# Performance work log

Hardware: AMD Instinct MI355X
Metric: run time of the kernel (lower is better)

## Reference

```python
import jax, jax.numpy as jnp
import numpy as np
import math

D_MODEL = 512
N_HEADS = 8
D_HEAD = D_MODEL // N_HEADS
B, T = 2, 2048


def quant_linear(x, W, b, bitwidth):
    # BitNet-b1.58 style: ternary weights (per-tensor absmean scale),
    # activations quantized to signed `bitwidth` with per-token absmax scale.
    ws = jnp.mean(jnp.abs(W)) + 1e-5
    Wq = jnp.clip(jnp.round(W / ws), -1.0, 1.0)
    Qb = 2.0 ** (bitwidth - 1) - 1.0
    xs = Qb / (jnp.max(jnp.abs(x), axis=-1, keepdims=True) + 1e-5)
    xq = jnp.clip(jnp.round(x * xs), -Qb, Qb)
    return (xq @ W.T if False else jnp.einsum('...i,oi->...o', xq, Wq)) * (ws / xs) + b


def layer_norm(x, g, b, eps=1e-5):
    mu = jnp.mean(x, axis=-1, keepdims=True)
    var = jnp.mean(jnp.square(x - mu), axis=-1, keepdims=True)
    return (x - mu) * jax.lax.rsqrt(var + eps) * g + b


def rel_shift(x):
    # x: [B, H, T, T]
    b, h, t1, t2 = x.shape
    x = jnp.pad(x, ((0, 0), (0, 0), (0, 0), (1, 0)))  # [B,H,T,T+1]
    x = x.reshape(b, h, t2 + 1, t1)[:, :, 1:, :]
    return x.reshape(b, h, t1, t2)


def setup_inputs() -> dict:
    key = jax.random.key(0)
    ks = jax.random.split(key, 16)
    s = 0.02
    inp = {
        'x': jax.random.normal(ks[0], (B, T, D_MODEL), jnp.float32),
        'mask': jnp.ones((B, T, T), jnp.int32),
        'pos_emb': jax.random.normal(ks[1], (1, T, D_MODEL), jnp.float32),
        'ln_g': jnp.ones((D_MODEL,), jnp.float32),
        'ln_b': jnp.zeros((D_MODEL,), jnp.float32),
        'Wq': jax.random.normal(ks[2], (D_MODEL, D_MODEL), jnp.float32) * s,
        'bq': jnp.zeros((D_MODEL,), jnp.float32),
        'Wk': jax.random.normal(ks[3], (D_MODEL, D_MODEL), jnp.float32) * s,
        'bk': jnp.zeros((D_MODEL,), jnp.float32),
        'Wv': jax.random.normal(ks[4], (D_MODEL, D_MODEL), jnp.float32) * s,
        'bv': jnp.zeros((D_MODEL,), jnp.float32),
        'Wp': jax.random.normal(ks[5], (D_MODEL, D_MODEL), jnp.float32) * s,
        'bp': jnp.zeros((D_MODEL,), jnp.float32),
        'Wo': jax.random.normal(ks[6], (D_MODEL, D_MODEL), jnp.float32) * s,
        'bo': jnp.zeros((D_MODEL,), jnp.float32),
        'pos_bias_u': jax.random.normal(ks[7], (N_HEADS, D_HEAD), jnp.float32) * 0.01,
        'pos_bias_v': jax.random.normal(ks[8], (N_HEADS, D_HEAD), jnp.float32) * 0.01,
        'bitwidth': 8,
    }
    return inp


def reference(x, mask, pos_emb, ln_g, ln_b, Wq, bq, Wk, bk, Wv, bv, Wp, bp, Wo, bo, pos_bias_u, pos_bias_v, bitwidth):
    b, t, c = x.shape
    y = layer_norm(x, ln_g, ln_b)
    # projections -> [B, H, T, Dh]
    Q = quant_linear(y, Wq, bq, bitwidth).reshape(b, t, N_HEADS, D_HEAD).transpose(0, 2, 1, 3)
    K = quant_linear(y, Wk, bk, bitwidth).reshape(b, t, N_HEADS, D_HEAD).transpose(0, 2, 1, 3)
    V = quant_linear(y, Wv, bv, bitwidth).reshape(b, t, N_HEADS, D_HEAD).transpose(0, 2, 1, 3)
    p = quant_linear(pos_emb, Wp, bp, bitwidth).reshape(1, t, N_HEADS, D_HEAD).transpose(0, 2, 1, 3)
    Qu = Q + pos_bias_u[None, :, None, :]
    Qv = Q + pos_bias_v[None, :, None, :]
    matrix_ac = jnp.einsum('bhqd,bhkd->bhqk', Qu, K)
    matrix_bd = rel_shift(jnp.einsum('bhqd,xhkd->bhqk', Qv, p))
    scores = (matrix_ac + matrix_bd) / math.sqrt(D_HEAD)
    scores = jnp.where(mask[:, None, :, :] == 0, -jnp.inf, scores)
    A = jnp.nan_to_num(jax.nn.softmax(scores, axis=-1), nan=0.0)
    H = jnp.einsum('bhqk,bhkd->bhqd', A, V).transpose(0, 2, 1, 3).reshape(b, t, c)
    H = quant_linear(H, Wo, bo, bitwidth)
    H = H * mask[:, :, 0:1].astype(H.dtype)  # seq mask
    return x + H
```

## Files before the change

kernel.cpp:

```cpp
#include <hip/hip_runtime.h>
#include <math.h>

#define TT 2048
#define DMODEL 512
#define NHEADS 8
#define DHEAD 64
#define NBATCH 2
#define MTOK (NBATCH*TT)
#define NSPLIT 4
#define SC 0.18033688011112042f
#define PADQ 68

typedef unsigned short u16;
typedef unsigned int u32;
typedef __bf16 bf16x8 __attribute__((ext_vector_type(8)));
typedef float f32x4 __attribute__((ext_vector_type(4)));
typedef float f32x2 __attribute__((ext_vector_type(2)));
typedef short s16x4 __attribute__((ext_vector_type(4)));
typedef short s16x8 __attribute__((ext_vector_type(8)));
typedef unsigned short u16x4 __attribute__((ext_vector_type(4)));
typedef unsigned int u32x4 __attribute__((ext_vector_type(4)));
typedef int s32x4 __attribute__((ext_vector_type(4)));

#define MFMA16(a,b,c) __builtin_amdgcn_mfma_f32_16x16x32_bf16(a,b,c,0,0,0)
#define MFMA_PV(a,b,c) __builtin_amdgcn_mfma_f32_16x16x16bf16_1k(a,b,c,0,0,0)

__device__ __forceinline__ u16 f2b(float f){
  u32 x = __float_as_uint(f);
  x = x + 0x7fffu + ((x >> 16) & 1u);
  return (u16)(x >> 16);
}
__device__ __forceinline__ float b2f(u16 u){
  return __uint_as_float(((u32)u) << 16);
}
__device__ __forceinline__ u32 cvtpk(float lo, float hi){
  u32 d; asm("v_cvt_pk_bf16_f32 %0, %1, %2" : "=v"(d) : "v"(lo), "v"(hi)); return d;
}
__device__ __forceinline__ u32 pk4fp8(float a, float b, float c, float d){
  u32 lo, hi;
  asm("v_cvt_pk_fp8_f32 %0, %1, %2" : "=v"(lo) : "v"(a), "v"(b));
  asm("v_cvt_pk_fp8_f32 %0, %1, %2" : "=v"(hi) : "v"(c), "v"(d));
  return (lo & 0xFFFFu) | (hi << 16);
}
__device__ __forceinline__ f32x2 upk2fp8(u32 v){
  f32x2 r;
  asm("v_cvt_pk_f32_fp8 %0, %1" : "=v"(r) : "v"(v));
  return r;
}
__device__ __forceinline__ size_t fidx(int t, int d){
  return ((size_t)((t>>4)*16 + (d>>5)))*512
       + (size_t)(((((d>>3)&3)*16) + (t&15))*8 + (d&7));
}

__global__ __launch_bounds__(256) void wprep1_kernel(
    const float* __restrict__ W0, const float* __restrict__ W1,
    const float* __restrict__ W2, const float* __restrict__ W3,
    const float* __restrict__ W4, float* __restrict__ partial)
{
  int widx = blockIdx.y;
  const float* W = (widx==0)?W0:(widx==1)?W1:(widx==2)?W2:(widx==3)?W3:W4;
  size_t base = (size_t)blockIdx.x * 4096;
  int tid = threadIdx.x;
  float s = 0.f;
  for (int i = tid; i < 4096; i += 256) s += fabsf(W[base + i]);
  __shared__ float red[256];
  red[tid] = s; __syncthreads();
  for (int o = 128; o > 0; o >>= 1){ if (tid < o) red[tid] += red[tid+o]; __syncthreads(); }
  if (tid == 0) partial[widx*64 + blockIdx.x] = red[0];
}

__global__ __launch_bounds__(256) void wprep2_kernel(
    const float* __restrict__ W0, const float* __restrict__ W1,
    const float* __restrict__ W2, const float* __restrict__ W3,
    const float* __restrict__ W4, const float* __restrict__ partial,
    float* __restrict__ wsv, u16* __restrict__ wt)
{
  int widx = blockIdx.y;
  const float* W = (widx==0)?W0:(widx==1)?W1:(widx==2)?W2:(widx==3)?W3:W4;
  __shared__ float red[64];
  int tid = threadIdx.x;
  if (tid < 64) red[tid] = partial[widx*64 + tid];
  __syncthreads();
  for (int o = 32; o > 0; o >>= 1){ if (tid < o) red[tid] += red[tid+o]; __syncthreads(); }
  float ws = red[0] * (1.0f/262144.0f) + 1e-5f;
  if (blockIdx.x == 0 && tid == 0) wsv[widx] = ws;
  int base = blockIdx.x * 1024;
  for (int i = tid; i < 1024; i += 256){
    int idx = base + i;
    int n = idx >> 9, k = idx & 511;
    float v = rintf(W[idx] / ws);
    v = fminf(fmaxf(v, -1.f), 1.f);
    wt[(size_t)widx*262144 + fidx(n, k)] = f2b(v);
  }
}

__global__ __launch_bounds__(256) void lnq_kernel(
    const float* __restrict__ x, const float* __restrict__ g, const float* __restrict__ b,
    const int* __restrict__ bwp, u16* __restrict__ xq, float* __restrict__ stok)
{
  int t = blockIdx.x;
  const float* xr = x + (size_t)t * DMODEL;
  int tid = threadIdx.x;
  float v0 = xr[tid], v1 = xr[tid + 256];
  __shared__ float red[256];
  red[tid] = v0 + v1; __syncthreads();
  for (int o=128;o>0;o>>=1){ if(tid<o) red[tid]+=red[tid+o]; __syncthreads(); }
  float mu = red[0] * (1.0f/512.0f);
  __syncthreads();
  float d0 = v0 - mu, d1 = v1 - mu;
  red[tid] = d0*d0 + d1*d1; __syncthreads();
  for (int o=128;o>0;o>>=1){ if(tid<o) red[tid]+=red[tid+o]; __syncthreads(); }
  float var = red[0] * (1.0f/512.0f);
  __syncthreads();
  float rs = rsqrtf(var + 1e-5f);
  float y0 = d0*rs*g[tid] + b[tid];
  float y1 = d1*rs*g[tid+256] + b[tid+256];
  red[tid] = fmaxf(fabsf(y0), fabsf(y1)); __syncthreads();
  for (int o=128;o>0;o>>=1){ if(tid<o) red[tid]=fmaxf(red[tid],red[tid+o]); __syncthreads(); }
  float amax = red[0];
  float Qb = (float)((1 << (bwp[0]-1)) - 1);
  float xs = Qb / (amax + 1e-5f);
  if (tid == 0) stok[t] = (amax + 1e-5f) / Qb;
  float q0 = fminf(fmaxf(rintf(y0 * xs), -Qb), Qb);
  float q1 = fminf(fmaxf(rintf(y1 * xs), -Qb), Qb);
  xq[fidx(t, tid)]       = f2b(q0);
  xq[fidx(t, tid + 256)] = f2b(q1);
}

__global__ __launch_bounds__(256) void quant_kernel(
    const float* __restrict__ src, const int* __restrict__ bwp,
    u16* __restrict__ xq, float* __restrict__ stok)
{
  int t = blockIdx.x;
  const float* xr = src + (size_t)t * DMODEL;
  int tid = threadIdx.x;
  float v0 = xr[tid], v1 = xr[tid + 256];
  __shared__ float red[256];
  red[tid] = fmaxf(fabsf(v0), fabsf(v1)); __syncthreads();
  for (int o=128;o>0;o>>=1){ if(tid<o) red[tid]=fmaxf(red[tid],red[tid+o]); __syncthreads(); }
  float amax = red[0];
  float Qb = (float)((1 << (bwp[0]-1)) - 1);
  float xs = Qb / (amax + 1e-5f);
  if (tid == 0) stok[t] = (amax + 1e-5f) / Qb;
  float q0 = fminf(fmaxf(rintf(v0 * xs), -Qb), Qb);
  float q1 = fminf(fmaxf(rintf(v1 * xs), -Qb), Qb);
  xq[fidx(t, tid)]       = f2b(q0);
  xq[fidx(t, tid + 256)] = f2b(q1);
}

__global__ __launch_bounds__(256) void maskflag_kernel(const int* __restrict__ mask, int* __restrict__ rowflag){
  int row = blockIdx.x;
  int tid = threadIdx.x;
  int ok = 1;
  const int* mr = mask + (size_t)row * TT;
  for (int i = tid; i < TT; i += 256) ok &= (mr[i] != 0);
  __shared__ int red[256];
  red[tid] = ok; __syncthreads();
  for (int o=128;o>0;o>>=1){ if(tid<o) red[tid] &= red[tid+o]; __syncthreads(); }
  if (tid == 0) rowflag[row] = red[0];
}

__global__ __launch_bounds__(256) void qkvgemm_kernel(
    const u16* __restrict__ Af, const u16* __restrict__ wtf,
    const float* __restrict__ stok, const float* __restrict__ wsv,
    const float* __restrict__ bq, const float* __restrict__ bk, const float* __restrict__ bv,
    const float* __restrict__ pbu, const float* __restrict__ pbv,
    u16* __restrict__ Qu, u16* __restrict__ Qv, u16* __restrict__ Kf, u16* __restrict__ Vf)
{
  int w = threadIdx.x >> 6, lane = threadIdx.x & 63;
  int g = lane >> 4, li = lane & 15;
  int mb = blockIdx.y*64 + w*16;
  int nb = blockIdx.x*64;
  int widx = nb >> 9;
  int ntb = (nb & 511) >> 4;
  f32x4 acc[4] = {{0,0,0,0},{0,0,0,0},{0,0,0,0},{0,0,0,0}};
  const u16* Ab = Af + (size_t)(mb >> 4)*16*512 + lane*8;
  const u16* Bb = wtf + (size_t)widx*262144 + (size_t)ntb*16*512 + lane*8;
  for (int kb = 0; kb < 16; kb++){
    bf16x8 a = *(const bf16x8*)(Ab + kb*512);
#pragma unroll
    for (int f = 0; f < 4; f++){
      bf16x8 bb = *(const bf16x8*)(Bb + (f*16 + kb)*512);
      acc[f] = MFMA16(a, bb, acc[f]);
    }
  }
  float ws = wsv[widx];
  const float* bias = (widx==0)?bq:(widx==1)?bk:bv;
  float sc[4];
#pragma unroll
  for (int r=0;r<4;r++) sc[r] = ws * stok[mb + 4*g + r];
#pragma unroll
  for (int f=0;f<4;f++){
    int n = nb + 16*f + li;
    int nq = n & 511;
    float bn = bias[nq];
#pragma unroll
    for (int r=0;r<4;r++){
      int m = mb + 4*g + r;
      float val = acc[f][r]*sc[r] + bn;
      int bb_ = m >> 11, t = m & (TT-1); int h = nq >> 6, d = nq & 63;
      int bh = bb_*NHEADS + h;
      if (widx == 0){
        size_t o = (((size_t)bh)*TT + t)*DHEAD + d;
        Qu[o] = f2b((val + pbu[nq])*SC);
        Qv[o] = f2b(val + pbv[nq]);
      } else if (widx == 1){
        size_t o = (((size_t)bh*128 + (t>>4))*2 + (d>>5))*512
                 + (size_t)((((d>>3)&3)*16 + (t&15))*8 + (d&7));
        Kf[o] = f2b(val);
      } else {
        size_t o = (((size_t)bh*128 + (t>>4))*2 + (d>>5))*512
                 + (size_t)(((((t>>2)&3)*16) + (d&15))*8 + (((d>>4)&1)*4) + (t&3));
        Vf[o] = f2b(val);
      }
    }
  }
}

template<int NF>
__global__ __launch_bounds__(256) void qgemm_kernel(
    const u16* __restrict__ Af, const u16* __restrict__ Wtf,
    const float* __restrict__ stok, const float* __restrict__ wsv, int widx,
    const float* __restrict__ bias, int mode,
    u16* __restrict__ outA, float* __restrict__ outF,
    const float* __restrict__ xin, const int* __restrict__ mask)
{
  int w = threadIdx.x >> 6, lane = threadIdx.x & 63;
  int g = lane >> 4, li = lane & 15;
  int mb = blockIdx.y*64 + w*16;
  int nb = blockIdx.x*(16*NF);
  f32x4 acc[NF];
#pragma unroll
  for (int f=0; f<NF; f++) acc[f] = (f32x4){0,0,0,0};
  const u16* Ab = Af + (size_t)(mb >> 4)*16*512 + lane*8;
  const u16* Bb = Wtf + (size_t)(nb >> 4)*16*512 + lane*8;
  for (int kb = 0; kb < 16; kb++){
    bf16x8 a = *(const bf16x8*)(Ab + kb*512);
#pragma unroll
    for (int f = 0; f < NF; f++){
      bf16x8 bb = *(const bf16x8*)(Bb + (f*16 + kb)*512);
      acc[f] = MFMA16(a, bb, acc[f]);
    }
  }
  float ws = wsv[widx];
  float sc[4];
#pragma unroll
  for (int r=0;r<4;r++) sc[r] = ws * stok[mb + 4*g + r];
#pragma unroll
  for (int f=0;f<NF;f++){
    int n = nb + 16*f + li;
    float bn = bias[n];
#pragma unroll
    for (int r=0;r<4;r++){
      int m = mb + 4*g + r;
      float val = acc[f][r]*sc[r] + bn;
      if (mode == 3){
        int h = n >> 6, d = n & 63;
        size_t o = (((size_t)h*128 + (m>>4))*2 + (d>>5))*512
                 + (size_t)((((d>>3)&3)*16 + (m&15))*8 + (d&7));
        outA[o] = f2b(val);
      } else {
        int bb_ = m >> 11, t = m & (TT-1);
        float mv = (float)mask[((size_t)bb_*TT + t)*TT];
        outF[(size_t)m*DMODEL + n] = xin[(size_t)m*DMODEL + n] + val*mv;
      }
    }
  }
}

__global__ __launch_bounds__(256) void bd_kernel(
    const u16* __restrict__ Qv, const u16* __restrict__ Pf, u32* __restrict__ bdq)
{
  __shared__ float lds[64*PADQ];
  int tid = threadIdx.x;
  int w = tid >> 6, lane = tid & 63;
  int g = lane >> 4, li = lane & 15;
  int bh = blockIdx.z, h = bh & 7;
  int qb = blockIdx.y*64, k0 = blockIdx.x*64;
  int qt = qb + 16*w;
  if (tid < 64){
    int kd = qb + tid + 1 - k0;
    if ((unsigned)kd < 64u) lds[kd*PADQ + tid] = 0.f;
  }
  const u16* Pbh = Pf + (size_t)h*128*1024;
  const u16* Qbh = Qv + (size_t)bh*TT*DHEAD;
  int qp = 16*w + 4*g;
  {
    const u16* qr = Qbh + (size_t)(qt + li)*DHEAD;
    bf16x8 a0 = *(const bf16x8*)(qr + 8*g);
    bf16x8 a1 = *(const bf16x8*)(qr + 32 + 8*g);
    int dkq = k0 - qt;
    for (int i = 0; i < 5; i++){
      if (dkq + 16*i > 15) break;
      int jt = k0 + TT - 16 - qt + 16*i;
      int j = jt + li;
      bool jok = (j <= TT-1);
      int jc = jok ? j : (TT-1);
      const u16* pr = Pbh + (size_t)(jc>>4)*1024 + (size_t)((g*16 + (jc&15))*8);
      f32x4 c = {0,0,0,0};
      c = MFMA16(a0, *(const bf16x8*)(pr),       c);
      c = MFMA16(a1, *(const bf16x8*)(pr + 512), c);
      int kp = 16*i - 15 + li + 4*g;
#pragma unroll
      for (int r = 0; r < 4; r++){
        int kpr = kp + r;
        if (jok && kpr >= 0 && kpr < 64)
          lds[kpr*PADQ + qp + r] = c[r]*SC;
      }
    }
  }
  {
    int q2r = qt + 1 + li; if (q2r > TT-1) q2r = TT-1;
    const u16* qr = Qbh + (size_t)q2r*DHEAD;
    bf16x8 a0 = *(const bf16x8*)(qr + 8*g);
    bf16x8 a1 = *(const bf16x8*)(qr + 32 + 8*g);
    int dqk = qt - k0;
    for (int i = 5; i >= 0; i--){
      if (16*i < dqk + 17) break;
      int jt2 = k0 - qt - 32 + 16*i;
      int j2 = jt2 + li;
      bool jok = (j2 >= 0);
      int jc = jok ? j2 : 0;
      const u16* pr = Pbh + (size_t)(jc>>4)*1024 + (size_t)((g*16 + (jc&15))*8);
      f32x4 c = {0,0,0,0};
      c = MFMA16(a0, *(const bf16x8*)(pr),       c);
      c = MFMA16(a1, *(const bf16x8*)(pr + 512), c);
      int kp = 16*i - 30 + li + 4*g;
#pragma unroll
      for (int r = 0; r < 4; r++){
        int kpr = kp + r;
        if (jok && kpr >= 0 && kpr < 64)
          lds[kpr*PADQ + qp + r] = c[r]*SC;
      }
    }
  }
  __syncthreads();
  {
    int kq = tid >> 4, qg = tid & 15;
    f32x4 v[4];
#pragma unroll
    for (int kk = 0; kk < 4; kk++)
      v[kk] = *(const f32x4*)(&lds[(4*kq + kk)*PADQ + 4*qg]);
    u32x4 o4;
#pragma unroll
    for (int qq = 0; qq < 4; qq++)
      o4[qq] = pk4fp8(v[0][qq], v[1][qq], v[2][qq], v[3][qq]);
    u32* ob = bdq + (size_t)bh*(TT/4)*TT + ((size_t)((k0>>2) + kq)*TT + qb + 4*qg);
    *(u32x4*)ob = o4;
  }
}

__global__ __launch_bounds__(256) void flash_kernel(
    const u16* __restrict__ Qu, const u16* __restrict__ Kf,
    const u16* __restrict__ Vf, const u32* __restrict__ bdq,
    const int* __restrict__ mask, const int* __restrict__ rowflag,
    u16* __restrict__ Opart, float* __restrict__ Mpart, float* __restrict__ Lpart)
{
  int w = threadIdx.x >> 6, lane = threadIdx.x & 63;
  int g = lane >> 4, li = lane & 15;
  int bh = blockIdx.y; int b = bh >> 3, h = bh & 7;
  int z = blockIdx.z;
  int qb = blockIdx.x*64 + w*16;
  int q = qb + li;

  const u16* qrow = Qu + ((size_t)bh*TT + q)*DHEAD;
  bf16x8 qu0 = *(const bf16x8*)(qrow + 8*g);
  bf16x8 qu1 = *(const bf16x8*)(qrow + 32 + 8*g);

  f32x4 acc[4] = {{0,0,0,0},{0,0,0,0},{0,0,0,0},{0,0,0,0}};
  float mrun = -3e38f, lrun = 0.f;
  int rf = rowflag[b*TT + q];
  bool needmask = (__all(rf) == 0);

  const u16* kfb = Kf + (size_t)bh*128*1024;
  const u16* vfb = Vf + (size_t)bh*128*1024;
  const u32* bdb = bdq + (size_t)bh*(TT/4)*TT;
  const int* maskq = mask + ((size_t)b*TT + q)*TT;

  int kbeg = z * (TT/NSPLIT);
  for (int k0 = kbeg; k0 < kbeg + TT/NSPLIT; k0 += 64){
    int kb = k0 >> 4;
    f32x4 s[4];
#pragma unroll
    for (int kc = 0; kc < 4; kc++){
      const u16* kp = kfb + (size_t)(kb + kc)*1024 + lane*8;
      f32x4 t_ = {0,0,0,0};
      t_ = MFMA16(*(const bf16x8*)(kp),       qu0, t_);
      t_ = MFMA16(*(const bf16x8*)(kp + 512), qu1, t_);
      s[kc] = t_;
    }
#pragma unroll
    for (int kc = 0; kc < 4; kc++){
      u32 wb = bdb[(size_t)((k0>>2) + 4*kc + g)*TT + q];
      f32x2 lo2 = upk2fp8(wb);
      f32x2 hi2 = upk2fp8(wb >> 16);
      s[kc][0] += lo2[0]; s[kc][1] += lo2[1];
      s[kc][2] += hi2[0]; s[kc][3] += hi2[1];
    }
    if (needmask && !rf){
#pragma unroll
      for (int kc = 0; kc < 4; kc++){
        s32x4 mv = *(const s32x4*)(maskq + k0 + 16*kc + 4*g);
#pragma unroll
        for (int r = 0; r < 4; r++)
          if (mv[r] == 0) s[kc][r] = -3e38f;
      }
    }
    float tm = s[0][0];
#pragma unroll
    for (int kc = 0; kc < 4; kc++)
#pragma unroll
      for (int r = 0; r < 4; r++) tm = fmaxf(tm, s[kc][r]);
    tm = fmaxf(tm, __shfl_xor(tm, 16));
    tm = fmaxf(tm, __shfl_xor(tm, 32));
    float mn;
    if (__all(tm <= mrun)){
      mn = mrun;
    } else {
      mn = fmaxf(mrun, tm);
      float fscq = __builtin_amdgcn_exp2f(mrun - mn);
      mrun = mn;
      lrun *= fscq;
#pragma unroll
      for (int r = 0; r < 4; r++){
        float fr = __shfl(fscq, 4*g + r);
        acc[0][r] *= fr; acc[1][r] *= fr; acc[2][r] *= fr; acc[3][r] *= fr;
      }
    }
    float ps = 0.f;
    s16x4 pk[4];
#pragma unroll
    for (int kc = 0; kc < 4; kc++){
      float p0 = __builtin_amdgcn_exp2f(s[kc][0] - mn);
      float p1 = __builtin_amdgcn_exp2f(s[kc][1] - mn);
      float p2 = __builtin_amdgcn_exp2f(s[kc][2] - mn);
      float p3 = __builtin_amdgcn_exp2f(s[kc][3] - mn);
      ps += (p0 + p1) + (p2 + p3);
      union { u32 w[2]; s16x4 v; } u_;
      u_.w[0] = cvtpk(p0, p1);
      u_.w[1] = cvtpk(p2, p3);
      pk[kc] = u_.v;
    }
    ps += __shfl_xor(ps, 16);
    ps += __shfl_xor(ps, 32);
    lrun += ps;
#pragma unroll
    for (int kc = 0; kc < 4; kc++){
      const u16* vp = vfb + (size_t)(kb + kc)*1024 + lane*8;
      bf16x8 v0 = *(const bf16x8*)(vp);
      bf16x8 v1 = *(const bf16x8*)(vp + 512);
      s16x8 w0 = (s16x8)v0, w1 = (s16x8)v1;
      acc[0] = MFMA_PV(pk[kc], __builtin_shufflevector(w0, w0, 0,1,2,3), acc[0]);
      acc[1] = MFMA_PV(pk[kc], __builtin_shufflevector(w0, w0, 4,5,6,7), acc[1]);
      acc[2] = MFMA_PV(pk[kc], __builtin_shufflevector(w1, w1, 0,1,2,3), acc[2]);
      acc[3] = MFMA_PV(pk[kc], __builtin_shufflevector(w1, w1, 4,5,6,7), acc[3]);
    }
  }
#pragma unroll
  for (int r = 0; r < 4; r++){
    size_t o = ((size_t)(b*TT + qb + 4*g + r)*NSPLIT + z)*DMODEL + h*DHEAD + li;
    Opart[o]      = f2b(acc[0][r]);
    Opart[o + 16] = f2b(acc[1][r]);
    Opart[o + 32] = f2b(acc[2][r]);
    Opart[o + 48] = f2b(acc[3][r]);
  }
  if (lane < 16){
    size_t mo = ((size_t)(b*TT + qb + li)*NSPLIT + z)*NHEADS + h;
    Mpart[mo] = mrun;
    Lpart[mo] = lrun;
  }
}

__global__ __launch_bounds__(256) void merge_kernel(
    const u16* __restrict__ Opart, const float* __restrict__ Mpart, const float* __restrict__ Lpart,
    const int* __restrict__ bwp, u16* __restrict__ xq, float* __restrict__ stok)
{
  int tok = blockIdx.x, tid = threadIdx.x;
  __shared__ float scl[NSPLIT][NHEADS];
  if (tid < NHEADS){
    int h = tid;
    float ms[NSPLIT], ls[NSPLIT];
#pragma unroll
    for (int s = 0; s < NSPLIT; s++){
      ms[s] = Mpart[((size_t)tok*NSPLIT + s)*NHEADS + h];
      ls[s] = Lpart[((size_t)tok*NSPLIT + s)*NHEADS + h];
    }
    float mst = ms[0];
#pragma unroll
    for (int s = 1; s < NSPLIT; s++) mst = fmaxf(mst, ms[s]);
    float sc_[NSPLIT]; float lst = 0.f;
#pragma unroll
    for (int s = 0; s < NSPLIT; s++){
      sc_[s] = __builtin_amdgcn_exp2f(ms[s] - mst);
      lst += ls[s]*sc_[s];
    }
    float inv = (lst > 0.f) ? 1.0f/lst : 0.f;
#pragma unroll
    for (int s = 0; s < NSPLIT; s++) scl[s][h] = sc_[s]*inv;
  }
  __syncthreads();
  float hv[2];
#pragma unroll
  for (int j = 0; j < 2; j++){
    int idx = tid + 256*j;
    int h = idx >> 6;
    float a = 0.f;
#pragma unroll
    for (int s = 0; s < NSPLIT; s++)
      a += b2f(Opart[((size_t)tok*NSPLIT + s)*DMODEL + idx]) * scl[s][h];
    hv[j] = a;
  }
  __shared__ float red[256];
  red[tid] = fmaxf(fabsf(hv[0]), fabsf(hv[1])); __syncthreads();
  for (int o=128;o>0;o>>=1){ if(tid<o) red[tid]=fmaxf(red[tid],red[tid+o]); __syncthreads(); }
  float amax = red[0];
  float Qb = (float)((1 << (bwp[0]-1)) - 1);
  float xs = Qb / (amax + 1e-5f);
  if (tid == 0) stok[tok] = (amax + 1e-5f) / Qb;
#pragma unroll
  for (int j = 0; j < 2; j++){
    int idx = tid + 256*j;
    float qv = fminf(fmaxf(rintf(hv[j] * xs), -Qb), Qb);
    xq[fidx(tok, idx)] = f2b(qv);
  }
}

extern "C" void kernel_launch(void* const* d_in, const int* in_sizes, int n_in,
                              void* d_out, int out_size, void* d_ws, size_t ws_size,
                              hipStream_t stream) {
  const float* x    = (const float*)d_in[0];
  const int*   mask = (const int*)  d_in[1];
  const float* pos  = (const float*)d_in[2];
  const float* lng  = (const float*)d_in[3];
  const float* lnb  = (const float*)d_in[4];
  const float* Wq   = (const float*)d_in[5];
  const float* bq   = (const float*)d_in[6];
  const float* Wk   = (const float*)d_in[7];
  const float* bk   = (const float*)d_in[8];
  const float* Wv   = (const float*)d_in[9];
  const float* bv   = (const float*)d_in[10];
  const float* Wp   = (const float*)d_in[11];
  const float* bp   = (const float*)d_in[12];
  const float* Wo   = (const float*)d_in[13];
  const float* bo   = (const float*)d_in[14];
  const float* pbu  = (const float*)d_in[15];
  const float* pbv  = (const float*)d_in[16];
  const int*   bwp  = (const int*)  d_in[17];
  float* out = (float*)d_out;

  char* wsb = (char*)d_ws;
  size_t off = 0;
  auto alloc = [&](size_t nbytes)->char* {
    char* p = wsb + off;
    off = (off + nbytes + 255) & ~(size_t)255;
    return p;
  };
  float* partial = (float*)alloc(5*64*sizeof(float));
  float* wsv     = (float*)alloc(5*sizeof(float));
  u16*   wt      = (u16*)  alloc((size_t)5*262144*2);
  float* stok_y  = (float*)alloc(MTOK*sizeof(float));
  float* stok_p  = (float*)alloc(TT*sizeof(float));
  u16*   Qu      = (u16*)  alloc((size_t)16*TT*DHEAD*2);
  u16*   Qv      = (u16*)  alloc((size_t)16*TT*DHEAD*2);
  u16*   Kf      = (u16*)  alloc((size_t)16*TT*DHEAD*2);
  u16*   Vf      = (u16*)  alloc((size_t)16*TT*DHEAD*2);
  u16*   pool    = (u16*)  alloc((size_t)MTOK*NSPLIT*DMODEL*2);
  u16*   xq_y    = pool;
  u16*   xq_p    = pool + (size_t)MTOK*DMODEL;
  u16*   Pf      = xq_p + (size_t)TT*DMODEL;
  u16*   Opart   = pool;
  float* Mpart   = (float*)alloc((size_t)MTOK*NSPLIT*NHEADS*sizeof(float));
  float* Lpart   = (float*)alloc((size_t)MTOK*NSPLIT*NHEADS*sizeof(float));
  u16*   xq_H    = (u16*)  alloc((size_t)MTOK*DMODEL*2);
  float* stok_H  = (float*)alloc(MTOK*sizeof(float));
  int*   rowflag = (int*)  alloc(MTOK*sizeof(int));
  u32*   bdq     = (u32*)  alloc((size_t)16*(TT/4)*TT*4);
  if (off > ws_size) return;

  wprep1_kernel<<<dim3(64,5), 256, 0, stream>>>(Wq, Wk, Wv, Wp, Wo, partial);
  wprep2_kernel<<<dim3(256,5), 256, 0, stream>>>(Wq, Wk, Wv, Wp, Wo, partial, wsv, wt);
  lnq_kernel<<<MTOK, 256, 0, stream>>>(x, lng, lnb, bwp, xq_y, stok_y);
  quant_kernel<<<TT, 256, 0, stream>>>(pos, bwp, xq_p, stok_p);
  maskflag_kernel<<<MTOK, 256, 0, stream>>>(mask, rowflag);
  qkvgemm_kernel<<<dim3(24,64), 256, 0, stream>>>(xq_y, wt, stok_y, wsv, bq, bk, bv, pbu, pbv,
                                                  Qu, Qv, Kf, Vf);
  qgemm_kernel<2><<<dim3(16,32), 256, 0, stream>>>(xq_p, wt + (size_t)3*262144, stok_p, wsv, 3, bp, 3,
                                                   Pf, nullptr, nullptr, nullptr);
  bd_kernel<<<dim3(32,32,16), 256, 0, stream>>>(Qv, Pf, bdq);
  flash_kernel<<<dim3(32,16,NSPLIT), 256, 0, stream>>>(Qu, Kf, Vf, bdq, mask, rowflag,
                                                       Opart, Mpart, Lpart);
  merge_kernel<<<MTOK, 256, 0, stream>>>(Opart, Mpart, Lpart, bwp, xq_H, stok_H);
  qgemm_kernel<2><<<dim3(16,64), 256, 0, stream>>>(xq_H, wt + (size_t)4*262144, stok_H, wsv, 4, bo, 4,
                                                   nullptr, out, x, mask);
}
```

Baseline: 182.1 us.

## Use wave shuffles for reductions, halve KV split, remap bd blocks, defer max shuffle

Replaces LDS tree reductions in the weight prep, layernorm/quant, mask-flag and merge kernels with wavefront shuffle reductions plus a four-entry cross-wave combine. Layernorm now computes variance in one pass as E[x^2]-mu^2. The mask-flag kernel uses vectorized loads and __all. The flash-attention KV split drops from 4 to 2, which halves the grid and the merge work but gives each block a longer KV loop. The bd kernel uses a 1D grid with a head-interleaved block mapping, and the flash kernel only does the cross-lane max shuffle when the running max actually changes. The one-pass variance is less numerically robust.

After: 175.3 us. -3.7%, faster.

```diff
diff --git a/kernel.cpp b/kernel.cpp
--- a/kernel.cpp
+++ b/kernel.cpp
@@ -7,7 +7,7 @@
 #define DHEAD 64
 #define NBATCH 2
 #define MTOK (NBATCH*TT)
-#define NSPLIT 4
+#define NSPLIT 2
 #define SC 0.18033688011112042f
 #define PADQ 68
 
@@ -60,13 +60,15 @@
   int widx = blockIdx.y;
   const float* W = (widx==0)?W0:(widx==1)?W1:(widx==2)?W2:(widx==3)?W3:W4;
   size_t base = (size_t)blockIdx.x * 4096;
-  int tid = threadIdx.x;
+  int tid = threadIdx.x, w = tid >> 6, lane = tid & 63;
   float s = 0.f;
   for (int i = tid; i < 4096; i += 256) s += fabsf(W[base + i]);
-  __shared__ float red[256];
-  red[tid] = s; __syncthreads();
-  for (int o = 128; o > 0; o >>= 1){ if (tid < o) red[tid] += red[tid+o]; __syncthreads(); }
-  if (tid == 0) partial[widx*64 + blockIdx.x] = red[0];
+#pragma unroll
+  for (int o = 1; o < 64; o <<= 1) s += __shfl_xor(s, o);
+  __shared__ float red[4];
+  if (lane == 0) red[w] = s;
+  __syncthreads();
+  if (tid == 0) partial[widx*64 + blockIdx.x] = red[0]+red[1]+red[2]+red[3];
 }
 
 __global__ __launch_bounds__(256) void wprep2_kernel(
@@ -100,24 +102,27 @@
 {
   int t = blockIdx.x;
   const float* xr = x + (size_t)t * DMODEL;
-  int tid = threadIdx.x;
+  int tid = threadIdx.x, w = tid >> 6, lane = tid & 63;
   float v0 = xr[tid], v1 = xr[tid + 256];
-  __shared__ float red[256];
-  red[tid] = v0 + v1; __syncthreads();
-  for (int o=128;o>0;o>>=1){ if(tid<o) red[tid]+=red[tid+o]; __syncthreads(); }
-  float mu = red[0] * (1.0f/512.0f);
-  __syncthreads();
-  float d0 = v0 - mu, d1 = v1 - mu;
-  red[tid] = d0*d0 + d1*d1; __syncthreads();
-  for (int o=128;o>0;o>>=1){ if(tid<o) red[tid]+=red[tid+o]; __syncthreads(); }
-  float var = red[0] * (1.0f/512.0f);
-  __syncthreads();
+  float s1 = v0 + v1, s2 = v0*v0 + v1*v1;
+#pragma unroll
+  for (int o = 1; o < 64; o <<= 1){ s1 += __shfl_xor(s1, o); s2 += __shfl_xor(s2, o); }
+  __shared__ float pa[4], pb[4], pm[4];
+  if (lane == 0){ pa[w] = s1; pb[w] = s2; }
+  __syncthreads();
+  float sum = pa[0]+pa[1]+pa[2]+pa[3];
+  float sqs = pb[0]+pb[1]+pb[2]+pb[3];
+  float mu  = sum * (1.0f/512.0f);
+  float var = sqs * (1.0f/512.0f) - mu*mu;
   float rs = rsqrtf(var + 1e-5f);
-  float y0 = d0*rs*g[tid] + b[tid];
-  float y1 = d1*rs*g[tid+256] + b[tid+256];
-  red[tid] = fmaxf(fabsf(y0), fabsf(y1)); __syncthreads();
-  for (int o=128;o>0;o>>=1){ if(tid<o) red[tid]=fmaxf(red[tid],red[tid+o]); __syncthreads(); }
-  float amax = red[0];
+  float y0 = (v0 - mu)*rs*g[tid] + b[tid];
+  float y1 = (v1 - mu)*rs*g[tid+256] + b[tid+256];
+  float am = fmaxf(fabsf(y0), fabsf(y1));
+#pragma unroll
+  for (int o = 1; o < 64; o <<= 1) am = fmaxf(am, __shfl_xor(am, o));
+  if (lane == 0) pm[w] = am;
+  __syncthreads();
+  float amax = fmaxf(fmaxf(pm[0], pm[1]), fmaxf(pm[2], pm[3]));
   float Qb = (float)((1 << (bwp[0]-1)) - 1);
   float xs = Qb / (amax + 1e-5f);
   if (tid == 0) stok[t] = (amax + 1e-5f) / Qb;
@@ -133,12 +138,15 @@
 {
   int t = blockIdx.x;
   const float* xr = src + (size_t)t * DMODEL;
-  int tid = threadIdx.x;
+  int tid = threadIdx.x, w = tid >> 6, lane = tid & 63;
   float v0 = xr[tid], v1 = xr[tid + 256];
-  __shared__ float red[256];
-  red[tid] = fmaxf(fabsf(v0), fabsf(v1)); __syncthreads();
-  for (int o=128;o>0;o>>=1){ if(tid<o) red[tid]=fmaxf(red[tid],red[tid+o]); __syncthreads(); }
-  float amax = red[0];
+  float am = fmaxf(fabsf(v0), fabsf(v1));
+#pragma unroll
+  for (int o = 1; o < 64; o <<= 1) am = fmaxf(am, __shfl_xor(am, o));
+  __shared__ float pm[4];
+  if (lane == 0) pm[w] = am;
+  __syncthreads();
+  float amax = fmaxf(fmaxf(pm[0], pm[1]), fmaxf(pm[2], pm[3]));
   float Qb = (float)((1 << (bwp[0]-1)) - 1);
   float xs = Qb / (amax + 1e-5f);
   if (tid == 0) stok[t] = (amax + 1e-5f) / Qb;
@@ -150,14 +158,15 @@
 
 __global__ __launch_bounds__(256) void maskflag_kernel(const int* __restrict__ mask, int* __restrict__ rowflag){
   int row = blockIdx.x;
-  int tid = threadIdx.x;
-  int ok = 1;
-  const int* mr = mask + (size_t)row * TT;
-  for (int i = tid; i < TT; i += 256) ok &= (mr[i] != 0);
-  __shared__ int red[256];
-  red[tid] = ok; __syncthreads();
-  for (int o=128;o>0;o>>=1){ if(tid<o) red[tid] &= red[tid+o]; __syncthreads(); }
-  if (tid == 0) rowflag[row] = red[0];
+  int tid = threadIdx.x, w = tid >> 6, lane = tid & 63;
+  const s32x4* mr = (const s32x4*)(mask + (size_t)row * TT);
+  s32x4 a = mr[tid], b2 = mr[tid + 256];
+  bool ok = (a[0]!=0)&(a[1]!=0)&(a[2]!=0)&(a[3]!=0)&(b2[0]!=0)&(b2[1]!=0)&(b2[2]!=0)&(b2[3]!=0);
+  int wok = __all(ok);
+  __shared__ int red[4];
+  if (lane == 0) red[w] = wok;
+  __syncthreads();
+  if (tid == 0) rowflag[row] = red[0] & red[1] & red[2] & red[3];
 }
 
 __global__ __launch_bounds__(256) void qkvgemm_kernel(
@@ -272,11 +281,16 @@
     const u16* __restrict__ Qv, const u16* __restrict__ Pf, u32* __restrict__ bdq)
 {
   __shared__ float lds[64*PADQ];
+  int L = blockIdx.x;
+  int m = L >> 3;
+  int bh = (L & 7) + 8*(m >> 10);
+  int inner = m & 1023;
+  int qb = (inner & 31) << 6;
+  int k0 = (inner >> 5) << 6;
+  int h = bh & 7;
   int tid = threadIdx.x;
   int w = tid >> 6, lane = tid & 63;
   int g = lane >> 4, li = lane & 15;
-  int bh = blockIdx.z, h = bh & 7;
-  int qb = blockIdx.y*64, k0 = blockIdx.x*64;
   int qt = qb + 16*w;
   if (tid < 64){
     int kd = qb + tid + 1 - k0;
@@ -411,12 +425,12 @@
     for (int kc = 0; kc < 4; kc++)
 #pragma unroll
       for (int r = 0; r < 4; r++) tm = fmaxf(tm, s[kc][r]);
-    tm = fmaxf(tm, __shfl_xor(tm, 16));
-    tm = fmaxf(tm, __shfl_xor(tm, 32));
     float mn;
     if (__all(tm <= mrun)){
       mn = mrun;
     } else {
+      tm = fmaxf(tm, __shfl_xor(tm, 16));
+      tm = fmaxf(tm, __shfl_xor(tm, 32));
       mn = fmaxf(mrun, tm);
       float fscq = __builtin_amdgcn_exp2f(mrun - mn);
       mrun = mn;
@@ -475,7 +489,7 @@
     const u16* __restrict__ Opart, const float* __restrict__ Mpart, const float* __restrict__ Lpart,
     const int* __restrict__ bwp, u16* __restrict__ xq, float* __restrict__ stok)
 {
-  int tok = blockIdx.x, tid = threadIdx.x;
+  int tok = blockIdx.x, tid = threadIdx.x, w = tid >> 6, lane = tid & 63;
   __shared__ float scl[NSPLIT][NHEADS];
   if (tid < NHEADS){
     int h = tid;
@@ -510,10 +524,13 @@
       a += b2f(Opart[((size_t)tok*NSPLIT + s)*DMODEL + idx]) * scl[s][h];
     hv[j] = a;
   }
-  __shared__ float red[256];
-  red[tid] = fmaxf(fabsf(hv[0]), fabsf(hv[1])); __syncthreads();
-  for (int o=128;o>0;o>>=1){ if(tid<o) red[tid]=fmaxf(red[tid],red[tid+o]); __syncthreads(); }
-  float amax = red[0];
+  float am = fmaxf(fabsf(hv[0]), fabsf(hv[1]));
+#pragma unroll
+  for (int o = 1; o < 64; o <<= 1) am = fmaxf(am, __shfl_xor(am, o));
+  __shared__ float pm[4];
+  if (lane == 0) pm[w] = am;
+  __syncthreads();
+  float amax = fmaxf(fmaxf(pm[0], pm[1]), fmaxf(pm[2], pm[3]));
   float Qb = (float)((1 << (bwp[0]-1)) - 1);
   float xs = Qb / (amax + 1e-5f);
   if (tid == 0) stok[tok] = (amax + 1e-5f) / Qb;
@@ -586,7 +603,7 @@
                                                   Qu, Qv, Kf, Vf);
   qgemm_kernel<2><<<dim3(16,32), 256, 0, stream>>>(xq_p, wt + (size_t)3*262144, stok_p, wsv, 3, bp, 3,
                                                    Pf, nullptr, nullptr, nullptr);
-  bd_kernel<<<dim3(32,32,16), 256, 0, stream>>>(Qv, Pf, bdq);
+  bd_kernel<<<16384, 256, 0, stream>>>(Qv, Pf, bdq);
   flash_kernel<<<dim3(32,16,NSPLIT), 256, 0, stream>>>(Qu, Kf, Vf, bdq, mask, rowflag,
                                                        Opart, Mpart, Lpart);
   merge_kernel<<<MTOK, 256, 0, stream>>>(Opart, Mpart, Lpart, bwp, xq_H, stok_H);
```
